# Kernel tuning notes

Hardware: AMD Instinct MI355X
Metric: run time of the kernel (lower is better)

The kernel has to match this reference:

```python
import jax, jax.numpy as jnp
import numpy as np

N, D = 32768, 512          # rows, input dim (row count 32-aligned per source)
C, K = 16, 16              # ncodebooks, codewords per codebook (4-bit codes)
S = D // C                 # subvector length per codebook
M = 1024                   # output columns (W_test.shape[1])


def setup_inputs() -> dict:
    key = jax.random.key(0)
    k1, k2, k3 = jax.random.split(key, 3)
    X = jax.random.normal(k1, (N, D), dtype=jnp.float32)
    protos = jax.random.normal(k2, (C, K, S), dtype=jnp.float32)
    luts = jax.random.normal(k3, (C, K, M), dtype=jnp.float32)
    return {"X": X, "protos": protos, "luts": luts}


def reference(X, protos, luts):
    n, d = X.shape
    c, k, s = protos.shape
    # --- PQ encode: nearest prototype per codebook subvector ---
    Xr = X.reshape(n, c, s)                                   # [N, C, S]
    dots = jnp.einsum("ncs,cks->nck", Xr, protos)             # [N, C, K]
    dists = (protos * protos).sum(-1)[None, :, :] - 2.0 * dots
    codes = jnp.argmin(dists, axis=-1)                        # [N, C] int codes
    # --- LUT gather-accumulate: out[n,m] = sum_c luts[c, codes[n,c], m] ---
    onehot = jax.nn.one_hot(codes, k, dtype=luts.dtype)       # [N, C, K]
    out = jnp.einsum("nck,ckm->nm", onehot, luts)             # [N, M]
    # forward() scales the approximate product by mean(X)
    return out * jnp.mean(X)
```

## Files before the change

kernel.cpp:

```cpp
#include <hip/hip_runtime.h>
#include <hip/hip_bf16.h>
#include <stdint.h>

#define N_ROWS 32768
#define DIM    512
#define CB     16
#define KW     16
#define SV     32
#define MCOLS  1024


__global__ __launch_bounds__(256) void prep_kernel(
    const float* __restrict__ protos, double* __restrict__ protos_d,
    double* __restrict__ norms_d)
{
    const int ck = threadIdx.x;
    const float* src = protos + (size_t)ck * SV;
    double* dst = protos_d + (size_t)ck * SV;
    double nk = 0.0;
    #pragma unroll
    for (int j = 0; j < SV; ++j) {
        double v = (double)src[j];
        dst[j] = v;
        nk += v * v;
    }
    norms_d[ck] = nk;
}

__global__ __launch_bounds__(256) void encode_kernel(
    const float* __restrict__ X, const double* __restrict__ protos_d,
    const double* __restrict__ norms_d, uint8_t* __restrict__ codes,
    double* __restrict__ sum_out)
{
    __shared__ double redsum[4];

    const int tid  = threadIdx.x;
    const int lane = tid & 63;
    const int wv   = tid >> 6;
    const int task = blockIdx.x * 4 + wv;
    const int c    = __builtin_amdgcn_readfirstlane(task & 15);
    const int row  = (task >> 4) * 64 + lane;

    const float* xp = X + (size_t)row * DIM + c * SV;
    double xd[SV];
    double sx = 0.0;
    #pragma unroll
    for (int j = 0; j < 8; ++j) {
        float4 v = *(const float4*)(xp + j * 4);
        xd[j * 4 + 0] = (double)v.x; xd[j * 4 + 1] = (double)v.y;
        xd[j * 4 + 2] = (double)v.z; xd[j * 4 + 3] = (double)v.w;
        sx += (double)v.x + (double)v.y + (double)v.z + (double)v.w;
    }

    const double* __restrict__ Pd = protos_d + (size_t)c * (KW * SV);
    const double* __restrict__ Nd = norms_d + (size_t)c * KW;

    double best = 1e300;
    int bk = 0;
    #pragma unroll
    for (int k = 0; k < KW; ++k) {
        double d0 = 0.0, d1 = 0.0;
        #pragma unroll
        for (int s2 = 0; s2 < SV / 2; ++s2) {
            d0 += xd[2 * s2]     * Pd[k * SV + 2 * s2];
            d1 += xd[2 * s2 + 1] * Pd[k * SV + 2 * s2 + 1];
        }
        double dist = Nd[k] - 2.0 * (d0 + d1);
        if (dist < best) { best = dist; bk = k; }
    }
    codes[(size_t)row * CB + c] = (uint8_t)bk;

    #pragma unroll
    for (int off = 32; off > 0; off >>= 1) sx += __shfl_down(sx, off);
    if (lane == 0) redsum[wv] = sx;
    __syncthreads();
    if (tid == 0) {
        double s = redsum[0] + redsum[1] + redsum[2] + redsum[3];
        atomicAdd(sum_out, s);
    }
}

__device__ __forceinline__ float bflo(uint32_t u) { return __uint_as_float(u << 16); }
__device__ __forceinline__ float bfhi(uint32_t u) { return __uint_as_float(u & 0xffff0000u); }

__device__ __forceinline__ uint32_t pack_bf16x2(float lo, float hi) {
    __hip_bfloat16 a = __float2bfloat16(lo);
    __hip_bfloat16 b = __float2bfloat16(hi);
    return (uint32_t)(*(const uint16_t*)&a) | ((uint32_t)(*(const uint16_t*)&b) << 16);
}

__global__ __launch_bounds__(512) void lut_accum_kernel(
    const float* __restrict__ luts, const uint8_t* __restrict__ codes,
    const double* __restrict__ sum_in, float* __restrict__ out)
{
    __shared__ uint16_t lut_s[CB * KW * 64];

    const int tid   = threadIdx.x;
    const int mtile = blockIdx.x & 15;
    const int nblk  = blockIdx.x >> 4;
    const int m0 = mtile * 64;
    const int n0 = nblk * 512;

    const float scale = (float)(sum_in[0] * (1.0 / ((double)N_ROWS * (double)DIM)));

    #pragma unroll
    for (int it = 0; it < 4; ++it) {
        const int chunk = it * 512 + tid;
        const int ck = chunk >> 3;
        const int m  = (chunk & 7) * 8;
        const float* src = luts + (size_t)ck * MCOLS + m0 + m;
        float4 a = *(const float4*)(src);
        float4 b = *(const float4*)(src + 4);
        uint4 p;
        p.x = pack_bf16x2(a.x * scale, a.y * scale);
        p.y = pack_bf16x2(a.z * scale, a.w * scale);
        p.z = pack_bf16x2(b.x * scale, b.y * scale);
        p.w = pack_bf16x2(b.z * scale, b.w * scale);
        ((uint4*)lut_s)[chunk] = p;
    }
    __syncthreads();

    const int mg   = tid & 7;
    const int rsub = tid >> 3;

    #pragma unroll
    for (int pass = 0; pass < 8; ++pass) {
        const int n = n0 + pass * 64 + rsub;
        const uint4 pk = *(const uint4*)(codes + (size_t)n * CB);
        const uint32_t w[4] = { pk.x, pk.y, pk.z, pk.w };

        float acc[8];
        #pragma unroll
        for (int j = 0; j < 8; ++j) acc[j] = 0.0f;

        #pragma unroll
        for (int c = 0; c < CB; ++c) {
            const uint32_t k = (w[c >> 2] >> ((c & 3) * 8)) & 15u;
            const uint16_t* ptr = lut_s + (((uint32_t)(c * KW) + k) << 6) + (mg << 3);
            const uint4 d = *(const uint4*)ptr;
            acc[0] += bflo(d.x); acc[1] += bfhi(d.x);
            acc[2] += bflo(d.y); acc[3] += bfhi(d.y);
            acc[4] += bflo(d.z); acc[5] += bfhi(d.z);
            acc[6] += bflo(d.w); acc[7] += bfhi(d.w);
        }

        float* op = out + (size_t)n * MCOLS + m0 + mg * 8;
        *(float4*)op       = make_float4(acc[0], acc[1], acc[2], acc[3]);
        *((float4*)op + 1) = make_float4(acc[4], acc[5], acc[6], acc[7]);
    }
}

extern "C" void kernel_launch(void* const* d_in, const int* in_sizes, int n_in,
                              void* d_out, int out_size, void* d_ws, size_t ws_size,
                              hipStream_t stream) {
    const float* X      = (const float*)d_in[0];
    const float* protos = (const float*)d_in[1];
    const float* luts   = (const float*)d_in[2];
    float* out = (float*)d_out;

    double*  sum_ws   = (double*)d_ws;
    double*  protos_d = (double*)((uint8_t*)d_ws + 256);
    double*  norms_d  = (double*)((uint8_t*)d_ws + 66048);
    uint8_t* codes    = (uint8_t*)d_ws + 68352;

    hipMemsetAsync(d_ws, 0, 8, stream);

    prep_kernel<<<dim3(1), dim3(256), 0, stream>>>(protos, protos_d, norms_d);

    encode_kernel<<<dim3(2048), dim3(256), 0, stream>>>(X, protos_d, norms_d,
                                                        codes, sum_ws);

    lut_accum_kernel<<<dim3(1024), dim3(512), 0, stream>>>(luts, codes, sum_ws, out);
}
```

Baseline: 229.1 us.

## Replace LUT gather-accumulate with one-hot bf16 MFMA and restructure encode mapping

The LUT accumulation kernel now builds one-hot bf16 fragments from the 4-bit codes through a small shared table and multiplies them against a transposed bf16 LUT tile in shared memory using 16x16x32 MFMA instructions. This replaces the scalar shared-memory gather and add loop. Codes are staged into shared memory, and output is written as scattered scalar stores per MFMA lane. The encode kernel now maps one codebook per block with four independent accumulators, and prep uses coalesced copies. The risks are uncoalesced scalar output stores and bank conflicts on the transposed LUT staging.

```diff
diff --git a/kernel.cpp b/kernel.cpp
--- a/kernel.cpp
+++ b/kernel.cpp
@@ -1,6 +1,7 @@
 #include <hip/hip_runtime.h>
 #include <hip/hip_bf16.h>
 #include <stdint.h>
+#include <string.h>
 
 #define N_ROWS 32768
 #define DIM    512
@@ -9,25 +10,30 @@
 #define SV     32
 #define MCOLS  1024
 
+#define LROW   264
+
+typedef __attribute__((ext_vector_type(8))) short bf16x8_t;
+typedef __attribute__((ext_vector_type(4))) float f32x4_t;
+
 
 __global__ __launch_bounds__(256) void prep_kernel(
     const float* __restrict__ protos, double* __restrict__ protos_d,
     double* __restrict__ norms_d)
 {
-    const int ck = threadIdx.x;
-    const float* src = protos + (size_t)ck * SV;
-    double* dst = protos_d + (size_t)ck * SV;
+    const int tid = threadIdx.x;
+    #pragma unroll
+    for (int j = 0; j < 32; ++j) {
+        const int idx = j * 256 + tid;
+        protos_d[idx] = (double)protos[idx];
+    }
+    const float* src = protos + tid * SV;
     double nk = 0.0;
     #pragma unroll
-    for (int j = 0; j < SV; ++j) {
-        double v = (double)src[j];
-        dst[j] = v;
-        nk += v * v;
-    }
-    norms_d[ck] = nk;
-}
-
-__global__ __launch_bounds__(256) void encode_kernel(
+    for (int j = 0; j < SV; ++j) { double v = (double)src[j]; nk += v * v; }
+    norms_d[tid] = nk;
+}
+
+__global__ __launch_bounds__(256, 4) void encode_kernel(
     const float* __restrict__ X, const double* __restrict__ protos_d,
     const double* __restrict__ norms_d, uint8_t* __restrict__ codes,
     double* __restrict__ sum_out)
@@ -37,9 +43,8 @@
     const int tid  = threadIdx.x;
     const int lane = tid & 63;
     const int wv   = tid >> 6;
-    const int task = blockIdx.x * 4 + wv;
-    const int c    = __builtin_amdgcn_readfirstlane(task & 15);
-    const int row  = (task >> 4) * 64 + lane;
+    const int c    = blockIdx.x & 15;
+    const int row  = (blockIdx.x >> 4) * 256 + tid;
 
     const float* xp = X + (size_t)row * DIM + c * SV;
     double xd[SV];
@@ -59,13 +64,16 @@
     int bk = 0;
     #pragma unroll
     for (int k = 0; k < KW; ++k) {
-        double d0 = 0.0, d1 = 0.0;
-        #pragma unroll
-        for (int s2 = 0; s2 < SV / 2; ++s2) {
-            d0 += xd[2 * s2]     * Pd[k * SV + 2 * s2];
-            d1 += xd[2 * s2 + 1] * Pd[k * SV + 2 * s2 + 1];
+        const double* pk = Pd + k * SV;
+        double d0 = 0.0, d1 = 0.0, d2 = 0.0, d3 = 0.0;
+        #pragma unroll
+        for (int s = 0; s < 8; ++s) {
+            d0 += xd[4 * s + 0] * pk[4 * s + 0];
+            d1 += xd[4 * s + 1] * pk[4 * s + 1];
+            d2 += xd[4 * s + 2] * pk[4 * s + 2];
+            d3 += xd[4 * s + 3] * pk[4 * s + 3];
         }
-        double dist = Nd[k] - 2.0 * (d0 + d1);
+        double dist = Nd[k] - 2.0 * ((d0 + d1) + (d2 + d3));
         if (dist < best) { best = dist; bk = k; }
     }
     codes[(size_t)row * CB + c] = (uint8_t)bk;
@@ -80,20 +88,13 @@
     }
 }
 
-__device__ __forceinline__ float bflo(uint32_t u) { return __uint_as_float(u << 16); }
-__device__ __forceinline__ float bfhi(uint32_t u) { return __uint_as_float(u & 0xffff0000u); }
-
-__device__ __forceinline__ uint32_t pack_bf16x2(float lo, float hi) {
-    __hip_bfloat16 a = __float2bfloat16(lo);
-    __hip_bfloat16 b = __float2bfloat16(hi);
-    return (uint32_t)(*(const uint16_t*)&a) | ((uint32_t)(*(const uint16_t*)&b) << 16);
-}
-
-__global__ __launch_bounds__(512) void lut_accum_kernel(
+__global__ __launch_bounds__(256, 4) void lut_mfma_kernel(
     const float* __restrict__ luts, const uint8_t* __restrict__ codes,
     const double* __restrict__ sum_in, float* __restrict__ out)
 {
-    __shared__ uint16_t lut_s[CB * KW * 64];
+    __shared__ uint16_t lut_s[64 * LROW];
+    __shared__ uint8_t  codes_s[512 * 16];
+    __shared__ uint4    tbl[32];
 
     const int tid   = threadIdx.x;
     const int mtile = blockIdx.x & 15;
@@ -103,50 +104,88 @@
 
     const float scale = (float)(sum_in[0] * (1.0 / ((double)N_ROWS * (double)DIM)));
 
-    #pragma unroll
-    for (int it = 0; it < 4; ++it) {
-        const int chunk = it * 512 + tid;
-        const int ck = chunk >> 3;
-        const int m  = (chunk & 7) * 8;
-        const float* src = luts + (size_t)ck * MCOLS + m0 + m;
-        float4 a = *(const float4*)(src);
-        float4 b = *(const float4*)(src + 4);
-        uint4 p;
-        p.x = pack_bf16x2(a.x * scale, a.y * scale);
-        p.y = pack_bf16x2(a.z * scale, a.w * scale);
-        p.z = pack_bf16x2(b.x * scale, b.y * scale);
-        p.w = pack_bf16x2(b.z * scale, b.w * scale);
-        ((uint4*)lut_s)[chunk] = p;
+    if (tid < 32) {
+        const int sel = tid >> 4, code = tid & 15;
+        const int t = code - sel * 8;
+        uint32_t d[4] = {0u, 0u, 0u, 0u};
+        if (t >= 0 && t < 8) d[t >> 1] = 0x3F80u << ((t & 1) * 16);
+        tbl[tid] = make_uint4(d[0], d[1], d[2], d[3]);
+    }
+
+    {
+        const uint4* src = (const uint4*)(codes + (size_t)n0 * CB);
+        uint4* dst = (uint4*)codes_s;
+        dst[tid]       = src[tid];
+        dst[tid + 256] = src[tid + 256];
+    }
+
+    for (int i = tid; i < 256 * 64; i += 256) {
+        const int ck = i >> 6, m = i & 63;
+        float v = luts[(size_t)ck * MCOLS + m0 + m] * scale;
+        __hip_bfloat16 b = __float2bfloat16(v);
+        lut_s[m * LROW + ck] = *(const uint16_t*)&b;
     }
     __syncthreads();
 
-    const int mg   = tid & 7;
-    const int rsub = tid >> 3;
-
-    #pragma unroll
-    for (int pass = 0; pass < 8; ++pass) {
-        const int n = n0 + pass * 64 + rsub;
-        const uint4 pk = *(const uint4*)(codes + (size_t)n * CB);
-        const uint32_t w[4] = { pk.x, pk.y, pk.z, pk.w };
-
-        float acc[8];
-        #pragma unroll
-        for (int j = 0; j < 8; ++j) acc[j] = 0.0f;
-
-        #pragma unroll
-        for (int c = 0; c < CB; ++c) {
-            const uint32_t k = (w[c >> 2] >> ((c & 3) * 8)) & 15u;
-            const uint16_t* ptr = lut_s + (((uint32_t)(c * KW) + k) << 6) + (mg << 3);
-            const uint4 d = *(const uint4*)ptr;
-            acc[0] += bflo(d.x); acc[1] += bfhi(d.x);
-            acc[2] += bflo(d.y); acc[3] += bfhi(d.y);
-            acc[4] += bflo(d.z); acc[5] += bfhi(d.z);
-            acc[6] += bflo(d.w); acc[7] += bfhi(d.w);
+    const int wv   = tid >> 6;
+    const int lane = tid & 63;
+    const int mloc = lane & 15;
+    const int half = lane >> 4;
+    const int sel  = half & 1;
+    const int h2   = half >> 1;
+    const int shiftbase = h2 * 8;
+
+    #pragma unroll
+    for (int rtq = 0; rtq < 2; ++rtq) {
+        const int rowbase = wv * 128 + rtq * 64;
+
+        uint4 crow[4];
+        #pragma unroll
+        for (int rt = 0; rt < 4; ++rt)
+            crow[rt] = *(const uint4*)(codes_s + (rowbase + rt * 16 + mloc) * 16);
+
+        f32x4_t acc[4][4];
+        #pragma unroll
+        for (int rt = 0; rt < 4; ++rt)
+            #pragma unroll
+            for (int ct = 0; ct < 4; ++ct)
+                acc[rt][ct] = (f32x4_t){0.f, 0.f, 0.f, 0.f};
+
+        #pragma unroll
+        for (int ki = 0; ki < 8; ++ki) {
+            bf16x8_t bf[4];
+            #pragma unroll
+            for (int ct = 0; ct < 4; ++ct) {
+                const uint16_t* bp = lut_s + (ct * 16 + mloc) * LROW
+                                   + ki * 32 + half * 8;
+                bf[ct] = *reinterpret_cast<const bf16x8_t*>(bp);
+            }
+            #pragma unroll
+            for (int rt = 0; rt < 4; ++rt) {
+                const uint32_t cws[4] = {crow[rt].x, crow[rt].y,
+                                         crow[rt].z, crow[rt].w};
+                const uint32_t code =
+                    (cws[ki >> 1] >> (shiftbase + (ki & 1) * 16)) & 0xffu;
+                const bf16x8_t af =
+                    *reinterpret_cast<const bf16x8_t*>(&tbl[sel * 16 + code]);
+                #pragma unroll
+                for (int ct = 0; ct < 4; ++ct)
+                    acc[rt][ct] = __builtin_amdgcn_mfma_f32_16x16x32_bf16(
+                        af, bf[ct], acc[rt][ct], 0, 0, 0);
+            }
         }
 
-        float* op = out + (size_t)n * MCOLS + m0 + mg * 8;
-        *(float4*)op       = make_float4(acc[0], acc[1], acc[2], acc[3]);
-        *((float4*)op + 1) = make_float4(acc[4], acc[5], acc[6], acc[7]);
+        #pragma unroll
+        for (int rt = 0; rt < 4; ++rt) {
+            const int grow = n0 + rowbase + rt * 16 + half * 4;
+            #pragma unroll
+            for (int reg = 0; reg < 4; ++reg) {
+                float* op = out + (size_t)(grow + reg) * MCOLS + m0 + mloc;
+                #pragma unroll
+                for (int ct = 0; ct < 4; ++ct)
+                    op[ct * 16] = acc[rt][ct][reg];
+            }
+        }
     }
 }
 
@@ -170,5 +209,5 @@
     encode_kernel<<<dim3(2048), dim3(256), 0, stream>>>(X, protos_d, norms_d,
                                                         codes, sum_ws);
 
-    lut_accum_kernel<<<dim3(1024), dim3(512), 0, stream>>>(luts, codes, sum_ws, out);
-}
+    lut_mfma_kernel<<<dim3(1024), dim3(256), 0, stream>>>(luts, codes, sum_ws, out);
+}
```

Measured after the change: 222.9 us. 1.03x faster.
